# Performance work log

Measured on AMD Instinct MI355X. Metric: run time of the kernel, lower is better.

## Reference

```python
import jax, jax.numpy as jnp
import numpy as np

N = 50000   # nodes per graph
E = 500000  # edges per graph
F_IN = 128  # num_features
H = 128     # hidden_channels
C = 64      # num_classes
G = 64      # graphs per batch
NEG_SLOPE = 0.2


def setup_inputs() -> dict:
    key = jax.random.key(0)
    ks = jax.random.split(key, 16)
    s = 1.0 / np.sqrt(H)
    return {
        "x1": jax.random.normal(ks[0], (N, F_IN), jnp.float32),
        "x2": jax.random.normal(ks[1], (N, F_IN), jnp.float32),
        # stacked params for the 2 GATConv layers (F_IN == H so shapes match)
        "convW": jax.random.normal(ks[2], (2, H, H), jnp.float32) * s,
        "att_src": jax.random.normal(ks[3], (2, H), jnp.float32) * s,
        "att_dst": jax.random.normal(ks[4], (2, H), jnp.float32) * s,
        "conv_b": jnp.zeros((2, H), jnp.float32),
        "mlp_w1": jax.random.normal(ks[5], (H, H), jnp.float32) * s,
        "mlp_b1": jnp.zeros((H,), jnp.float32),
        "mlp_w2": jax.random.normal(ks[6], (H, C), jnp.float32) * s,
        "mlp_b2": jnp.zeros((C,), jnp.float32),
        "edge_index1": jax.random.randint(ks[7], (2, E), 0, N, jnp.int64),
        "batch1": jnp.sort(jax.random.randint(ks[8], (N,), 0, G, jnp.int64)),
        "edge_index2": jax.random.randint(ks[9], (2, E), 0, N, jnp.int64),
        "batch2": jnp.sort(jax.random.randint(ks[10], (N,), 0, G, jnp.int64)),
    }


def gat_conv(x, src, dst, W, a_s, a_d, b):
    # PyG GATConv, heads=1, add_self_loops already applied in src/dst
    n = x.shape[0]
    h = x @ W                                   # [N, H]
    alpha_s = h @ a_s                           # [N]
    alpha_d = h @ a_d                           # [N]
    e = alpha_s[src] + alpha_d[dst]             # [Etot]
    e = jnp.where(e > 0, e, NEG_SLOPE * e)      # leaky_relu
    # segment softmax over incoming edges of each dst node
    m = jax.ops.segment_max(e, dst, num_segments=n)
    ex = jnp.exp(e - m[dst])
    denom = jax.ops.segment_sum(ex, dst, num_segments=n)
    alpha = ex / denom[dst]                     # [Etot]
    out = jax.ops.segment_sum(h[src] * alpha[:, None], dst, num_segments=n)
    return out + b


def reference(x1, x2, convW, att_src, att_dst, conv_b,
              mlp_w1, mlp_b1, mlp_w2, mlp_b2,
              edge_index1, batch1, edge_index2, batch2):
    def branch(x, ei):
        n = x.shape[0]
        loops = jnp.arange(n, dtype=ei.dtype)
        src = jnp.concatenate([ei[0], loops])
        dst = jnp.concatenate([ei[1], loops])
        # num_layers=3 -> 2 convs; i != num_layers-1 always true -> ELU after each
        for l in range(2):
            x = gat_conv(x, src, dst, convW[l], att_src[l], att_dst[l], conv_b[l])
            x = jax.nn.elu(x)
            # dropout p=0.5 is identity in eval mode
        return jax.nn.relu(x @ mlp_w1 + mlp_b1) @ mlp_w2 + mlp_b2

    h1 = branch(x1, edge_index1)
    h2 = branch(x2, edge_index2)
    p1 = jax.ops.segment_sum(h1, batch1, num_segments=G)  # [G, C]
    p2 = jax.ops.segment_sum(h2, batch2, num_segments=G)  # [G, C]
    return p1.T @ p2                                      # [C, C]
```

## Files before the change

### kernel.cpp

```cpp
#include <hip/hip_runtime.h>
#include <cstdint>
#include <cstddef>

#define NNODES 50000
#define NEDGES 500000
#define NTOT (NEDGES + NNODES)
#define HDIM 128
#define CDIM 64
#define GDIM 64
#define NB 250
#define NPB 200
#define CHUNK 2048
#define NCHB ((NEDGES + CHUNK - 1) / CHUNK)

typedef __bf16 bf16x8 __attribute__((ext_vector_type(8)));
typedef __bf16 bf16x2 __attribute__((ext_vector_type(2)));
typedef float f32x4 __attribute__((ext_vector_type(4)));


__global__ __launch_bounds__(256) void k_setup(const float* __restrict__ convW,
                                               const float* __restrict__ w1,
                                               const float* __restrict__ w2,
                                               const float* __restrict__ a_s,
                                               const float* __restrict__ a_d,
                                               __bf16* __restrict__ WtC,
                                               __bf16* __restrict__ Wt1,
                                               __bf16* __restrict__ Wt2,
                                               float* __restrict__ Wa,
                                               float* __restrict__ p) {
    int b = blockIdx.x, tid = threadIdx.x;
    if (b < 128) {
        int i = b * 256 + tid;
        int mat = i >> 14, rem = i & 16383;
        int k = rem >> 7, n = rem & 127;
        WtC[mat * 16384 + n * 128 + k] = (__bf16)convW[i];
    } else if (b < 192) {
        int i = (b - 128) * 256 + tid;
        int k = i >> 7, n = i & 127;
        Wt1[n * 128 + k] = (__bf16)w1[i];
    } else if (b < 224) {
        int i = (b - 192) * 256 + tid;
        int k = i >> 6, n = i & 63;
        Wt2[n * 128 + k] = (__bf16)w2[i];
    } else if (b == 224) {
        for (int o = tid; o < 512; o += 256) {
            int l = o >> 8, r = o & 255;
            int type = r >> 7, k = r & 127;
            const float* a = (type ? a_d : a_s) + l * 128;
            const float* Wrow = convW + l * 16384 + k * 128;
            float s = 0.f;
            for (int j = 0; j < 128; j++) s += Wrow[j] * a[j];
            Wa[o] = s;
        }
    } else {
        for (int i = tid; i < 2 * GDIM * CDIM; i += 256) p[i] = 0.f;
    }
}


__global__ __launch_bounds__(256) void k_bhist(const int* __restrict__ ei0,
                                               const int* __restrict__ ei1,
                                               int* __restrict__ bcntB, int e) {
    __shared__ int h[NB];
    const int* dst = (blockIdx.y ? ei1 : ei0) + NEDGES;
    int* bcnt = bcntB + blockIdx.y * NB;
    for (int t = threadIdx.x; t < NB; t += 256) h[t] = 0;
    __syncthreads();
    int base = blockIdx.x * CHUNK;
    int lim = min(base + CHUNK, e);
    for (int i = base + threadIdx.x; i < lim; i += 256) atomicAdd(&h[dst[i] / NPB], 1);
    __syncthreads();
    for (int t = threadIdx.x; t < NB; t += 256)
        if (h[t]) atomicAdd(&bcnt[t], h[t]);
}

__global__ __launch_bounds__(256) void k_bscan(const int* __restrict__ bcntB,
                                               int* __restrict__ boffB,
                                               int* __restrict__ bcurB) {
    __shared__ int s[256];
    int t = threadIdx.x;
    const int* bcnt = bcntB + blockIdx.y * NB;
    int* boff = boffB + blockIdx.y * (NB + 1);
    int* bcur = bcurB + blockIdx.y * NB;
    int v = (t < NB) ? bcnt[t] : 0;
    s[t] = v;
    __syncthreads();
    for (int off = 1; off < 256; off <<= 1) {
        int x = (t >= off) ? s[t - off] : 0;
        __syncthreads();
        s[t] += x;
        __syncthreads();
    }
    if (t < NB) {
        boff[t + 1] = s[t];
        bcur[t] = s[t] - v;
        if (t == 0) boff[0] = 0;
    }
}

__global__ __launch_bounds__(256) void k_part(const int* __restrict__ ei0,
                                              const int* __restrict__ ei1,
                                              int* __restrict__ bcurB,
                                              int2* __restrict__ partB, int e) {
    __shared__ int cnt[NB], boffL[NB], gbase[NB], cur2[NB];
    __shared__ int tmp[256];
    __shared__ int2 staged[CHUNK];
    const int* eis = blockIdx.y ? ei1 : ei0;
    int* bcur = bcurB + blockIdx.y * NB;
    int2* part = partB + blockIdx.y * (size_t)NEDGES;
    int t = threadIdx.x;
    for (int i = t; i < NB; i += 256) { cnt[i] = 0; cur2[i] = 0; }
    __syncthreads();
    int base = blockIdx.x * CHUNK;
    int lim = min(base + CHUNK, e);
    int nloc = lim - base;

    int s_[8], d_[8], b_[8];
    bool v_[8];
#pragma unroll
    for (int k = 0; k < 8; k++) {
        int i = base + k * 256 + t;
        v_[k] = i < lim;
        s_[k] = 0; d_[k] = 0; b_[k] = 0;
        if (v_[k]) {
            s_[k] = eis[i];
            d_[k] = eis[NEDGES + i];
            b_[k] = d_[k] / NPB;
            atomicAdd(&cnt[b_[k]], 1);
        }
    }
    __syncthreads();
    tmp[t] = (t < NB) ? cnt[t] : 0;
    __syncthreads();
    for (int off = 1; off < 256; off <<= 1) {
        int x = (t >= off) ? tmp[t - off] : 0;
        __syncthreads();
        tmp[t] += x;
        __syncthreads();
    }
    if (t < NB) boffL[t] = tmp[t] - cnt[t];
    __syncthreads();
    if (t < NB) {
        int c = cnt[t];
        gbase[t] = c ? atomicAdd(&bcur[t], c) : 0;
    }
    __syncthreads();
#pragma unroll
    for (int k = 0; k < 8; k++) {
        if (v_[k]) {
            int pos = atomicAdd(&cur2[b_[k]], 1);
            staged[boffL[b_[k]] + pos] = make_int2(s_[k], d_[k]);
        }
    }
    __syncthreads();
    for (int i = t; i < nloc; i += 256) {
        int2 r = staged[i];
        int b = r.y / NPB;
        part[gbase[b] + (i - boffL[b])] = r;
    }
}

__global__ __launch_bounds__(256) void k_bdeg(const int2* __restrict__ partB,
                                              const int* __restrict__ boffB,
                                              int* __restrict__ degB, size_t sN) {
    __shared__ int h[NPB];
    int b = blockIdx.x;
    const int* boff = boffB + blockIdx.y * (NB + 1);
    const int2* part = partB + blockIdx.y * (size_t)NEDGES;
    int* deg = degB + blockIdx.y * sN;
    int t = threadIdx.x;
    if (t < NPB) h[t] = 0;
    __syncthreads();
    int beg = boff[b], end = boff[b + 1];
    int n0 = b * NPB;
    for (int i = beg + t; i < end; i += 256) atomicAdd(&h[part[i].y - n0], 1);
    __syncthreads();
    if (t < NPB) deg[n0 + t] = h[t];
}

__device__ inline int block_scan_incl(int v, int* lds) {
    int lane = threadIdx.x & 63, wid = threadIdx.x >> 6;
#pragma unroll
    for (int off = 1; off < 64; off <<= 1) {
        int nv = __shfl_up(v, off);
        if (lane >= off) v += nv;
    }
    if (lane == 63) lds[wid] = v;
    __syncthreads();
    if (wid == 0) {
        int s = (lane < 16) ? lds[lane] : 0;
#pragma unroll
        for (int off = 1; off < 16; off <<= 1) {
            int nv = __shfl_up(s, off);
            if (lane >= off) s += nv;
        }
        if (lane < 16) lds[lane] = s;
    }
    __syncthreads();
    return (wid > 0) ? v + lds[wid - 1] : v;
}

__global__ __launch_bounds__(1024) void k_scan1(const int* __restrict__ degB, int* __restrict__ inclB,
                                                int* __restrict__ bsumsB, size_t sN, int n) {
    __shared__ int lds[16];
    const int* deg = degB + blockIdx.y * sN;
    int* incl = inclB + blockIdx.y * sN;
    int* bsums = bsumsB + blockIdx.y * 64;
    int i = blockIdx.x * 1024 + threadIdx.x;
    int v = (i < n) ? deg[i] : 0;
    int s = block_scan_incl(v, lds);
    if (i < n) incl[i] = s;
    if (threadIdx.x == 1023) bsums[blockIdx.x] = s;
}

__global__ void k_scan2(int* __restrict__ bsumsB, int nb) {
    int* bsums = bsumsB + blockIdx.y * 64;
    int lane = threadIdx.x;
    int v = (lane < nb) ? bsums[lane] : 0;
#pragma unroll
    for (int off = 1; off < 64; off <<= 1) {
        int nv = __shfl_up(v, off);
        if (lane >= off) v += nv;
    }
    if (lane < nb) bsums[lane] = v;
}

__global__ __launch_bounds__(1024) void k_scan3(const int* __restrict__ inclB,
                                                const int* __restrict__ bsumsB, int* __restrict__ rpB,
                                                size_t sN, size_t sNp1, int n) {
    int i = blockIdx.x * 1024 + threadIdx.x;
    if (i >= n) return;
    const int* incl = inclB + blockIdx.y * sN;
    const int* bsums = bsumsB + blockIdx.y * 64;
    int* row_ptr = rpB + blockIdx.y * sNp1;
    int off = (blockIdx.x > 0) ? bsums[blockIdx.x - 1] : 0;
    row_ptr[i + 1] = incl[i] + off + i + 1;
    if (i == 0) row_ptr[0] = 0;
}

__global__ __launch_bounds__(256) void k_place(const int2* __restrict__ partB,
                                               const int* __restrict__ boffB,
                                               const int* __restrict__ rpB, size_t sNp1,
                                               int* __restrict__ colB, size_t sE) {
    __shared__ int cur[NPB];
    int b = blockIdx.x;
    const int* boff = boffB + blockIdx.y * (NB + 1);
    const int2* part = partB + blockIdx.y * (size_t)NEDGES;
    const int* row_ptr = rpB + blockIdx.y * sNp1;
    int* col = colB + blockIdx.y * sE;
    int t = threadIdx.x;
    int n0 = b * NPB;
    if (t < NPB) {
        int rp = row_ptr[n0 + t];
        cur[t] = rp + 1;
        col[rp] = n0 + t;
    }
    __syncthreads();
    int beg = boff[b], end = boff[b + 1];
    for (int i = beg + t; i < end; i += 256) {
        int2 r = part[i];
        int p = atomicAdd(&cur[r.y - n0], 1);
        col[p] = r.x;
    }
}


template <bool AF32>
__global__ __launch_bounds__(256) void k_gemm_conv(const float* __restrict__ x0,
                                                   const float* __restrict__ x1,
                                                   const __bf16* __restrict__ Ab, size_t As_,
                                                   const __bf16* __restrict__ Wt,
                                                   const float* __restrict__ Was,
                                                   const float* __restrict__ Wad,
                                                   float* __restrict__ asB, float* __restrict__ adB,
                                                   size_t aS,
                                                   __bf16* __restrict__ OutB, size_t Os_, int M) {
    constexpr int BN = 128;
    __shared__ __align__(16) unsigned short As[64][136];
    __shared__ __align__(16) unsigned short Bs[BN][136];
    const int tid = threadIdx.x;
    const int lane = tid & 63, w = tid >> 6;
    const int row0 = blockIdx.x * 64;
    __bf16* Out = OutB + blockIdx.y * Os_;

#pragma unroll
    for (int t = 0; t < 4; t++) {
        int ch = t * 256 + tid;
        int r = ch >> 4, cx = ch & 15;
        int grow = row0 + r;
        bf16x8 v = {};
        if (grow < M) {
            if (AF32) {
                const float* Ap = (blockIdx.y ? x1 : x0) + (size_t)grow * 128 + cx * 8;
                float4 f0 = *reinterpret_cast<const float4*>(Ap);
                float4 f1 = *reinterpret_cast<const float4*>(Ap + 4);
                v[0] = (__bf16)f0.x; v[1] = (__bf16)f0.y; v[2] = (__bf16)f0.z; v[3] = (__bf16)f0.w;
                v[4] = (__bf16)f1.x; v[5] = (__bf16)f1.y; v[6] = (__bf16)f1.z; v[7] = (__bf16)f1.w;
            } else {
                v = *reinterpret_cast<const bf16x8*>(Ab + blockIdx.y * As_ + (size_t)grow * 128 + cx * 8);
            }
        }
        *reinterpret_cast<bf16x8*>(&As[r][cx * 8]) = v;
    }
#pragma unroll
    for (int t = 0; t < 8; t++) {
        int ch = t * 256 + tid;
        int r = ch >> 4, cx = ch & 15;
        bf16x8 v = *reinterpret_cast<const bf16x8*>(Wt + (size_t)r * 128 + cx * 8);
        *reinterpret_cast<bf16x8*>(&Bs[r][cx * 8]) = v;
    }
    __syncthreads();

    {
        int row = tid >> 2, seg = tid & 3;
        float ss = 0.f, sd = 0.f;
#pragma unroll
        for (int k = 0; k < 32; k++) {
            int kk = seg * 32 + k;
            float a = __int_as_float(((unsigned)As[row][kk]) << 16);
            ss += a * Was[kk];
            sd += a * Wad[kk];
        }
        ss += __shfl_xor(ss, 1); ss += __shfl_xor(ss, 2);
        sd += __shfl_xor(sd, 1); sd += __shfl_xor(sd, 2);
        if (seg == 0) {
            int grow = row0 + row;
            if (grow < M) {
                (asB + blockIdx.y * aS)[grow] = ss;
                (adB + blockIdx.y * aS)[grow] = sd;
            }
        }
    }

    const int wr0 = (w >> 1) * 32;
    const int wc0 = (w & 1) * 64;
    f32x4 acc[2][4] = {};

#pragma unroll
    for (int ks = 0; ks < 4; ks++) {
        const int koff = ks * 32 + (lane >> 4) * 8;
        bf16x8 af[2], bfr[4];
#pragma unroll
        for (int mf = 0; mf < 2; mf++)
            af[mf] = *reinterpret_cast<const bf16x8*>(&As[wr0 + mf * 16 + (lane & 15)][koff]);
#pragma unroll
        for (int nf = 0; nf < 4; nf++)
            bfr[nf] = *reinterpret_cast<const bf16x8*>(&Bs[wc0 + nf * 16 + (lane & 15)][koff]);
#pragma unroll
        for (int mf = 0; mf < 2; mf++)
#pragma unroll
            for (int nf = 0; nf < 4; nf++)
                acc[mf][nf] = __builtin_amdgcn_mfma_f32_16x16x32_bf16(af[mf], bfr[nf], acc[mf][nf], 0, 0, 0);
    }

#pragma unroll
    for (int mf = 0; mf < 2; mf++) {
#pragma unroll
        for (int r = 0; r < 4; r++) {
            int row = row0 + wr0 + mf * 16 + (lane >> 4) * 4 + r;
            if (row >= M) continue;
#pragma unroll
            for (int nf = 0; nf < 4; nf++) {
                int colc = wc0 + nf * 16 + (lane & 15);
                Out[(size_t)row * BN + colc] = (__bf16)acc[mf][nf][r];
            }
        }
    }
}


__global__ __launch_bounds__(256) void k_gat_agg(const __bf16* __restrict__ hB, size_t hS,
                                                 const float* __restrict__ asB,
                                                 const float* __restrict__ adB, size_t aS,
                                                 const int* __restrict__ rpB, size_t sNp1,
                                                 const int* __restrict__ colB, size_t sE,
                                                 const float* __restrict__ bias,
                                                 __bf16* __restrict__ outB, size_t oS, int n) {
    int node = blockIdx.x * 4 + (threadIdx.x >> 6);
    int lane = threadIdx.x & 63;
    if (node >= n) return;
    const float* alpha_s = asB + blockIdx.y * aS;
    const int* row_ptr = rpB + blockIdx.y * sNp1;
    const int* col = colB + blockIdx.y * sE;
    const char* hbase = (const char*)(hB + blockIdx.y * hS);
    float ad = (adB + blockIdx.y * aS)[node];
    int beg = row_ptr[node], end = row_ptr[node + 1];
    int deg = end - beg;
    int sub = lane >> 4, fo = lane & 15;
    int foff = fo * 16;

    float acc[8] = {0.f, 0.f, 0.f, 0.f, 0.f, 0.f, 0.f, 0.f};

    if (deg <= 64) {
        bool v = lane < deg;
        int c = 0;
        float e = -1e30f;
        if (v) {
            c = col[beg + lane];
            e = alpha_s[c] + ad;
            e = (e > 0.f) ? e : 0.2f * e;
        }
        float m = e;
#pragma unroll
        for (int off = 32; off; off >>= 1) m = fmaxf(m, __shfl_xor(m, off));
        float ex = v ? __expf(e - m) : 0.f;
        float den = ex;
#pragma unroll
        for (int off = 32; off; off >>= 1) den += __shfl_xor(den, off);
        float wn = ex / den;

        int nIter = (deg + 3) >> 2;
        int k = sub;
        for (int t = 0; t < nIter; t += 2) {
            int k1 = k & 63, k2 = (k + 4) & 63;
            int c1 = __shfl(c, k1); float w1 = __shfl(wn, k1);
            int c2 = __shfl(c, k2); float w2 = __shfl(wn, k2);
            bool v1 = k < deg, v2 = (k + 4) < deg;
            w1 = v1 ? w1 : 0.f; c1 = v1 ? c1 : 0;
            w2 = v2 ? w2 : 0.f; c2 = v2 ? c2 : 0;
            bf16x8 h1 = *reinterpret_cast<const bf16x8*>(hbase + (c1 << 8) + foff);
            bf16x8 h2 = *reinterpret_cast<const bf16x8*>(hbase + (c2 << 8) + foff);
#pragma unroll
            for (int q = 0; q < 8; q++) acc[q] += w1 * (float)h1[q] + w2 * (float)h2[q];
            k += 8;
        }
    } else {
        float m = -1e30f;
        for (int i = beg + lane; i < end; i += 64) {
            float e = alpha_s[col[i]] + ad;
            e = (e > 0.f) ? e : 0.2f * e;
            m = fmaxf(m, e);
        }
#pragma unroll
        for (int off = 32; off; off >>= 1) m = fmaxf(m, __shfl_xor(m, off));
        float den = 0.f;
        for (int i = beg + lane; i < end; i += 64) {
            float e = alpha_s[col[i]] + ad;
            e = (e > 0.f) ? e : 0.2f * e;
            den += __expf(e - m);
        }
#pragma unroll
        for (int off = 32; off; off >>= 1) den += __shfl_xor(den, off);
        float rinv = 1.f / den;
        for (int i = beg + sub; i < end; i += 4) {
            int cc = col[i];
            float e = alpha_s[cc] + ad;
            e = (e > 0.f) ? e : 0.2f * e;
            float wv = __expf(e - m) * rinv;
            bf16x8 hv = *reinterpret_cast<const bf16x8*>(hbase + (cc << 8) + foff);
#pragma unroll
            for (int q = 0; q < 8; q++) acc[q] += wv * (float)hv[q];
        }
    }

#pragma unroll
    for (int q = 0; q < 8; q++) {
        acc[q] += __shfl_xor(acc[q], 16);
        acc[q] += __shfl_xor(acc[q], 32);
    }
    float2 bv = *reinterpret_cast<const float2*>(bias + fo * 8 + 2 * sub);
    float x0 = (sub & 2) ? ((sub & 1) ? acc[6] : acc[4]) : ((sub & 1) ? acc[2] : acc[0]);
    float x1 = (sub & 2) ? ((sub & 1) ? acc[7] : acc[5]) : ((sub & 1) ? acc[3] : acc[1]);
    x0 += bv.x; x1 += bv.y;
    x0 = (x0 > 0.f) ? x0 : __expf(x0) - 1.f;
    x1 = (x1 > 0.f) ? x1 : __expf(x1) - 1.f;
    bf16x2 ov;
    ov.x = (__bf16)x0; ov.y = (__bf16)x1;
    char* ob = (char*)(outB + blockIdx.y * oS) + ((unsigned)node << 8) + foff + sub * 4;
    *reinterpret_cast<unsigned int*>(ob) = __builtin_bit_cast(unsigned int, ov);
}


__global__ __launch_bounds__(256) void k_mlp_pool(const __bf16* __restrict__ AbB, size_t As_,
                                                  const __bf16* __restrict__ Wt1,
                                                  const __bf16* __restrict__ Wt2,
                                                  const float* __restrict__ b1,
                                                  const float* __restrict__ b2,
                                                  const int* __restrict__ bat0,
                                                  const int* __restrict__ bat1,
                                                  float* __restrict__ pB, size_t pS, int M) {
    __shared__ __align__(16) unsigned short As[64][136];
    __shared__ __align__(16) unsigned short Bs[128][136];
    const int tid = threadIdx.x;
    const int lane = tid & 63, w = tid >> 6;
    const int row0 = blockIdx.x * 64;
    const __bf16* Ab = AbB + blockIdx.y * As_;
    const int* batch = blockIdx.y ? bat1 : bat0;
    float* p = pB + blockIdx.y * pS;

#pragma unroll
    for (int t = 0; t < 4; t++) {
        int ch = t * 256 + tid;
        int r = ch >> 4, cx = ch & 15;
        int grow = row0 + r;
        bf16x8 v = {};
        if (grow < M) v = *reinterpret_cast<const bf16x8*>(Ab + (size_t)grow * 128 + cx * 8);
        *reinterpret_cast<bf16x8*>(&As[r][cx * 8]) = v;
    }
#pragma unroll
    for (int t = 0; t < 8; t++) {
        int ch = t * 256 + tid;
        int r = ch >> 4, cx = ch & 15;
        bf16x8 v = *reinterpret_cast<const bf16x8*>(Wt1 + (size_t)r * 128 + cx * 8);
        *reinterpret_cast<bf16x8*>(&Bs[r][cx * 8]) = v;
    }
    __syncthreads();

    {
        const int wr0 = (w >> 1) * 32;
        const int wc0 = (w & 1) * 64;
        f32x4 acc[2][4] = {};
#pragma unroll
        for (int ks = 0; ks < 4; ks++) {
            const int koff = ks * 32 + (lane >> 4) * 8;
            bf16x8 af[2], bfr[4];
#pragma unroll
            for (int mf = 0; mf < 2; mf++)
                af[mf] = *reinterpret_cast<const bf16x8*>(&As[wr0 + mf * 16 + (lane & 15)][koff]);
#pragma unroll
            for (int nf = 0; nf < 4; nf++)
                bfr[nf] = *reinterpret_cast<const bf16x8*>(&Bs[wc0 + nf * 16 + (lane & 15)][koff]);
#pragma unroll
            for (int mf = 0; mf < 2; mf++)
#pragma unroll
                for (int nf = 0; nf < 4; nf++)
                    acc[mf][nf] = __builtin_amdgcn_mfma_f32_16x16x32_bf16(af[mf], bfr[nf], acc[mf][nf], 0, 0, 0);
        }
        __syncthreads();
#pragma unroll
        for (int mf = 0; mf < 2; mf++)
#pragma unroll
            for (int r = 0; r < 4; r++) {
                int row = wr0 + mf * 16 + (lane >> 4) * 4 + r;
#pragma unroll
                for (int nf = 0; nf < 4; nf++) {
                    int colc = wc0 + nf * 16 + (lane & 15);
                    float v = fmaxf(acc[mf][nf][r] + b1[colc], 0.f);
                    As[row][colc] = __builtin_bit_cast(unsigned short, (__bf16)v);
                }
            }
#pragma unroll
        for (int t = 0; t < 4; t++) {
            int ch = t * 256 + tid;
            int r = ch >> 4, cx = ch & 15;
            bf16x8 v = *reinterpret_cast<const bf16x8*>(Wt2 + (size_t)r * 128 + cx * 8);
            *reinterpret_cast<bf16x8*>(&Bs[r][cx * 8]) = v;
        }
        __syncthreads();
    }

    const int wr2 = w * 16;
    f32x4 acc2[4] = {};
#pragma unroll
    for (int ks = 0; ks < 4; ks++) {
        const int koff = ks * 32 + (lane >> 4) * 8;
        bf16x8 a2 = *reinterpret_cast<const bf16x8*>(&As[wr2 + (lane & 15)][koff]);
#pragma unroll
        for (int nf = 0; nf < 4; nf++) {
            bf16x8 bf2 = *reinterpret_cast<const bf16x8*>(&Bs[nf * 16 + (lane & 15)][koff]);
            acc2[nf] = __builtin_amdgcn_mfma_f32_16x16x32_bf16(a2, bf2, acc2[nf], 0, 0, 0);
        }
    }

    int q = lane >> 4, c = lane & 15;
    bool full = (row0 + 63) < M;
    int g0 = batch[min(row0, M - 1)];
    int g1 = batch[min(row0 + 63, M - 1)];
    if (full && g0 == g1) {
        float s0 = acc2[0][0] + acc2[0][1] + acc2[0][2] + acc2[0][3];
        float s1 = acc2[1][0] + acc2[1][1] + acc2[1][2] + acc2[1][3];
        float s2 = acc2[2][0] + acc2[2][1] + acc2[2][2] + acc2[2][3];
        float s3 = acc2[3][0] + acc2[3][1] + acc2[3][2] + acc2[3][3];
        s0 += __shfl_xor(s0, 16); s0 += __shfl_xor(s0, 32);
        s1 += __shfl_xor(s1, 16); s1 += __shfl_xor(s1, 32);
        s2 += __shfl_xor(s2, 16); s2 += __shfl_xor(s2, 32);
        s3 += __shfl_xor(s3, 16); s3 += __shfl_xor(s3, 32);
        float v = (q & 2) ? ((q & 1) ? s3 : s2) : ((q & 1) ? s1 : s0);
        v += 16.f * b2[q * 16 + c];
        atomicAdd(&p[g0 * CDIM + q * 16 + c], v);
    } else {
        float b2v[4];
#pragma unroll
        for (int nf = 0; nf < 4; nf++) b2v[nf] = b2[nf * 16 + c];
#pragma unroll
        for (int r = 0; r < 4; r++) {
            int row = row0 + wr2 + q * 4 + r;
            if (row >= M) continue;
            int g = batch[row];
#pragma unroll
            for (int nf = 0; nf < 4; nf++)
                atomicAdd(&p[g * CDIM + nf * 16 + c], acc2[nf][r] + b2v[nf]);
        }
    }
}


__global__ __launch_bounds__(64) void k_final(const float* __restrict__ p, float* __restrict__ out) {
    int i = blockIdx.x;
    int j = threadIdx.x;
    const float* p1 = p;
    const float* p2 = p + GDIM * CDIM;
    float s = 0.f;
    for (int g = 0; g < GDIM; ++g) s += p1[g * CDIM + i] * p2[g * CDIM + j];
    out[i * CDIM + j] = s;
}


static inline size_t align_up(size_t x, size_t a) { return (x + a - 1) & ~(a - 1); }

struct Ws {
    __bf16 *Hb, *Yb;
    __bf16 *WtC, *Wt1, *Wt2;
    float *alpha_s, *alpha_d, *Wa, *p;
    int *deg, *incl, *row_ptr, *bsums, *col;
    int *bcnt, *boff, *bcur;
    int2* part;
    size_t sNH, sN, sNp1, sE;
    size_t need;
};

static Ws carve(void* ws, bool combined) {
    char* p = (char*)ws;
    size_t off = 0;
    Ws w;
    int nb = combined ? 2 : 1;
    auto take = [&](size_t bytes) {
        char* r = p + off;
        off = align_up(off + bytes, 256);
        return r;
    };
    w.Hb = (__bf16*)take((size_t)nb * NNODES * HDIM * 2);
    w.Yb = (__bf16*)take((size_t)nb * NNODES * HDIM * 2);
    w.alpha_s = (float*)take((size_t)nb * NNODES * 4);
    w.alpha_d = (float*)take((size_t)nb * NNODES * 4);
    w.col = (int*)take((size_t)nb * NTOT * 4);
    w.part = (int2*)take((size_t)nb * NEDGES * 8);
    w.deg = (int*)take((size_t)nb * NNODES * 4);
    w.incl = (int*)take((size_t)nb * NNODES * 4);
    w.row_ptr = (int*)take((size_t)nb * (NNODES + 1) * 4);
    w.bsums = (int*)take((size_t)2 * 64 * 4);
    w.bcnt = (int*)take((size_t)2 * NB * 4);
    w.boff = (int*)take((size_t)2 * (NB + 1) * 4);
    w.bcur = (int*)take((size_t)2 * NB * 4);
    w.WtC = (__bf16*)take((size_t)2 * HDIM * HDIM * 2);
    w.Wt1 = (__bf16*)take((size_t)HDIM * HDIM * 2);
    w.Wt2 = (__bf16*)take((size_t)HDIM * CDIM * 2);
    w.Wa = (float*)take((size_t)512 * 4);
    w.p = (float*)take((size_t)2 * GDIM * CDIM * 4);
    w.need = off;
    size_t s = combined ? 1 : 0;
    w.sNH = s * (size_t)NNODES * HDIM;
    w.sN = s * (size_t)NNODES;
    w.sNp1 = s * (size_t)(NNODES + 1);
    w.sE = s * (size_t)NTOT;
    return w;
}

static void pipeline(const Ws& w, const float* xA, const float* xB,
                     const int* eiA, const int* eiB,
                     const int* batA, const int* batB,
                     const float* conv_b, const float* b1, const float* b2,
                     float* pbase, size_t pstride, int yc, hipStream_t stream) {
    const int N = NNODES, E = NEDGES;
    int nb = (N + 1023) / 1024;
    dim3 gC(NCHB, yc), gB(NB, yc), g1(1, yc), gS(nb, yc);
    dim3 gW((N + 3) / 4, yc);
    dim3 gG((N + 63) / 64, yc);

    hipMemsetAsync(w.bcnt, 0, (size_t)yc * NB * 4, stream);
    k_bhist<<<gC, 256, 0, stream>>>(eiA, eiB, w.bcnt, E);
    k_bscan<<<g1, 256, 0, stream>>>(w.bcnt, w.boff, w.bcur);
    k_part<<<gC, 256, 0, stream>>>(eiA, eiB, w.bcur, w.part, E);
    k_bdeg<<<gB, 256, 0, stream>>>(w.part, w.boff, w.deg, w.sN);
    k_scan1<<<gS, 1024, 0, stream>>>(w.deg, w.incl, w.bsums, w.sN, N);
    k_scan2<<<g1, 64, 0, stream>>>(w.bsums, nb);
    k_scan3<<<gS, 1024, 0, stream>>>(w.incl, w.bsums, w.row_ptr, w.sN, w.sNp1, N);
    k_place<<<gB, 256, 0, stream>>>(w.part, w.boff, w.row_ptr, w.sNp1, w.col, w.sE);

    k_gemm_conv<true><<<gG, 256, 0, stream>>>(
        xA, xB, nullptr, 0, w.WtC, w.Wa, w.Wa + 128,
        w.alpha_s, w.alpha_d, w.sN, w.Hb, w.sNH, N);
    k_gat_agg<<<gW, 256, 0, stream>>>(w.Hb, w.sNH, w.alpha_s, w.alpha_d, w.sN,
                                      w.row_ptr, w.sNp1, w.col, w.sE, conv_b, w.Yb, w.sNH, N);
    k_gemm_conv<false><<<gG, 256, 0, stream>>>(
        nullptr, nullptr, w.Yb, w.sNH, w.WtC + HDIM * HDIM, w.Wa + 256, w.Wa + 384,
        w.alpha_s, w.alpha_d, w.sN, w.Hb, w.sNH, N);
    k_gat_agg<<<gW, 256, 0, stream>>>(w.Hb, w.sNH, w.alpha_s, w.alpha_d, w.sN,
                                      w.row_ptr, w.sNp1, w.col, w.sE, conv_b + HDIM, w.Yb, w.sNH, N);
    k_mlp_pool<<<gG, 256, 0, stream>>>(w.Yb, w.sNH, w.Wt1, w.Wt2, b1, b2,
                                       batA, batB, pbase, pstride, N);
}

extern "C" void kernel_launch(void* const* d_in, const int* in_sizes, int n_in, void* d_out,
                              int out_size, void* d_ws, size_t ws_size, hipStream_t stream) {
    const float* x1      = (const float*)d_in[0];
    const float* x2      = (const float*)d_in[1];
    const float* convW   = (const float*)d_in[2];
    const float* att_src = (const float*)d_in[3];
    const float* att_dst = (const float*)d_in[4];
    const float* conv_b  = (const float*)d_in[5];
    const float* mlp_w1  = (const float*)d_in[6];
    const float* mlp_b1  = (const float*)d_in[7];
    const float* mlp_w2  = (const float*)d_in[8];
    const float* mlp_b2  = (const float*)d_in[9];
    const int* ei1       = (const int*)d_in[10];
    const int* batch1    = (const int*)d_in[11];
    const int* ei2       = (const int*)d_in[12];
    const int* batch2    = (const int*)d_in[13];
    float* out = (float*)d_out;

    Ws wc = carve(d_ws, true);
    bool combined = ws_size >= wc.need;
    Ws w = combined ? wc : carve(d_ws, false);

    k_setup<<<226, 256, 0, stream>>>(convW, mlp_w1, mlp_w2, att_src, att_dst,
                                     w.WtC, w.Wt1, w.Wt2, w.Wa, w.p);

    if (combined) {
        pipeline(w, x1, x2, ei1, ei2, batch1, batch2, conv_b,
                 mlp_b1, mlp_b2, w.p, (size_t)GDIM * CDIM, 2, stream);
    } else {
        pipeline(w, x1, x1, ei1, ei1, batch1, batch1, conv_b,
                 mlp_b1, mlp_b2, w.p, 0, 1, stream);
        pipeline(w, x2, x2, ei2, ei2, batch2, batch2, conv_b,
                 mlp_b1, mlp_b2, w.p + GDIM * CDIM, 0, 1, stream);
    }

    k_final<<<CDIM, 64, 0, stream>>>(w.p, out);
}
```

Before: 347.0 us.

## Fuse CSR degree/scan/placement into one kernel and use 16-lane groups per node

Merges the degree histogram, three-pass global scan and edge placement into a single per-bucket kernel. The bucket offset from the partition scan serves as the global prefix, and a local block scan computes row pointers. This removes four launches and their intermediate buffers. Separately, GAT aggregation now gives each node a 16-lane group instead of a full wavefront, with each lane owning 8 features, which removes the cross-subgroup shuffle reduction but serializes edges per node.

```diff
diff --git a/kernel.cpp b/kernel.cpp
--- a/kernel.cpp
+++ b/kernel.cpp
@@ -160,106 +160,53 @@
     }
 }
 
-__global__ __launch_bounds__(256) void k_bdeg(const int2* __restrict__ partB,
-                                              const int* __restrict__ boffB,
-                                              int* __restrict__ degB, size_t sN) {
+__global__ __launch_bounds__(256) void k_place(const int2* __restrict__ partB,
+                                               const int* __restrict__ boffB,
+                                               int* __restrict__ rpB, size_t sNp1,
+                                               int* __restrict__ colB, size_t sE) {
     __shared__ int h[NPB];
+    __shared__ int lds4[4];
     int b = blockIdx.x;
     const int* boff = boffB + blockIdx.y * (NB + 1);
     const int2* part = partB + blockIdx.y * (size_t)NEDGES;
-    int* deg = degB + blockIdx.y * sN;
-    int t = threadIdx.x;
-    if (t < NPB) h[t] = 0;
-    __syncthreads();
-    int beg = boff[b], end = boff[b + 1];
-    int n0 = b * NPB;
-    for (int i = beg + t; i < end; i += 256) atomicAdd(&h[part[i].y - n0], 1);
-    __syncthreads();
-    if (t < NPB) deg[n0 + t] = h[t];
-}
-
-__device__ inline int block_scan_incl(int v, int* lds) {
-    int lane = threadIdx.x & 63, wid = threadIdx.x >> 6;
-#pragma unroll
-    for (int off = 1; off < 64; off <<= 1) {
-        int nv = __shfl_up(v, off);
-        if (lane >= off) v += nv;
-    }
-    if (lane == 63) lds[wid] = v;
-    __syncthreads();
-    if (wid == 0) {
-        int s = (lane < 16) ? lds[lane] : 0;
-#pragma unroll
-        for (int off = 1; off < 16; off <<= 1) {
-            int nv = __shfl_up(s, off);
-            if (lane >= off) s += nv;
-        }
-        if (lane < 16) lds[lane] = s;
-    }
-    __syncthreads();
-    return (wid > 0) ? v + lds[wid - 1] : v;
-}
-
-__global__ __launch_bounds__(1024) void k_scan1(const int* __restrict__ degB, int* __restrict__ inclB,
-                                                int* __restrict__ bsumsB, size_t sN, int n) {
-    __shared__ int lds[16];
-    const int* deg = degB + blockIdx.y * sN;
-    int* incl = inclB + blockIdx.y * sN;
-    int* bsums = bsumsB + blockIdx.y * 64;
-    int i = blockIdx.x * 1024 + threadIdx.x;
-    int v = (i < n) ? deg[i] : 0;
-    int s = block_scan_incl(v, lds);
-    if (i < n) incl[i] = s;
-    if (threadIdx.x == 1023) bsums[blockIdx.x] = s;
-}
-
-__global__ void k_scan2(int* __restrict__ bsumsB, int nb) {
-    int* bsums = bsumsB + blockIdx.y * 64;
-    int lane = threadIdx.x;
-    int v = (lane < nb) ? bsums[lane] : 0;
-#pragma unroll
-    for (int off = 1; off < 64; off <<= 1) {
-        int nv = __shfl_up(v, off);
-        if (lane >= off) v += nv;
-    }
-    if (lane < nb) bsums[lane] = v;
-}
-
-__global__ __launch_bounds__(1024) void k_scan3(const int* __restrict__ inclB,
-                                                const int* __restrict__ bsumsB, int* __restrict__ rpB,
-                                                size_t sN, size_t sNp1, int n) {
-    int i = blockIdx.x * 1024 + threadIdx.x;
-    if (i >= n) return;
-    const int* incl = inclB + blockIdx.y * sN;
-    const int* bsums = bsumsB + blockIdx.y * 64;
     int* row_ptr = rpB + blockIdx.y * sNp1;
-    int off = (blockIdx.x > 0) ? bsums[blockIdx.x - 1] : 0;
-    row_ptr[i + 1] = incl[i] + off + i + 1;
-    if (i == 0) row_ptr[0] = 0;
-}
-
-__global__ __launch_bounds__(256) void k_place(const int2* __restrict__ partB,
-                                               const int* __restrict__ boffB,
-                                               const int* __restrict__ rpB, size_t sNp1,
-                                               int* __restrict__ colB, size_t sE) {
-    __shared__ int cur[NPB];
-    int b = blockIdx.x;
-    const int* boff = boffB + blockIdx.y * (NB + 1);
-    const int2* part = partB + blockIdx.y * (size_t)NEDGES;
-    const int* row_ptr = rpB + blockIdx.y * sNp1;
     int* col = colB + blockIdx.y * sE;
     int t = threadIdx.x;
     int n0 = b * NPB;
+    if (t < NPB) h[t] = 0;
+    __syncthreads();
+    int beg = boff[b], end = boff[b + 1];
+    for (int i = beg + t; i < end; i += 256) atomicAdd(&h[part[i].y - n0], 1);
+    __syncthreads();
+    int v = (t < NPB) ? h[t] : 0;
+    int lane = t & 63, wid = t >> 6;
+    int incl = v;
+#pragma unroll
+    for (int off = 1; off < 64; off <<= 1) {
+        int nv = __shfl_up(incl, off);
+        if (lane >= off) incl += nv;
+    }
+    if (lane == 63) lds4[wid] = incl;
+    __syncthreads();
+    if (t == 0) {
+        int s = 0;
+#pragma unroll
+        for (int j = 0; j < 4; j++) { s += lds4[j]; lds4[j] = s; }
+    }
+    __syncthreads();
+    if (wid > 0) incl += lds4[wid - 1];
     if (t < NPB) {
-        int rp = row_ptr[n0 + t];
-        cur[t] = rp + 1;
-        col[rp] = n0 + t;
-    }
-    __syncthreads();
-    int beg = boff[b], end = boff[b + 1];
+        int rp_end = beg + n0 + incl + t + 1;
+        row_ptr[n0 + t + 1] = rp_end;
+        int rp_start = rp_end - v - 1;
+        col[rp_start] = n0 + t;
+        h[t] = rp_start + 1;
+        if (b == 0 && t == 0) row_ptr[0] = 0;
+    }
+    __syncthreads();
     for (int i = beg + t; i < end; i += 256) {
         int2 r = part[i];
-        int p = atomicAdd(&cur[r.y - n0], 1);
+        int p = atomicAdd(&h[r.y - n0], 1);
         col[p] = r.x;
     }
 }
@@ -376,8 +323,9 @@
                                                  const int* __restrict__ colB, size_t sE,
                                                  const float* __restrict__ bias,
                                                  __bf16* __restrict__ outB, size_t oS, int n) {
-    int node = blockIdx.x * 4 + (threadIdx.x >> 6);
-    int lane = threadIdx.x & 63;
+    int grp = threadIdx.x >> 4;
+    int node = blockIdx.x * 16 + grp;
+    int l = threadIdx.x & 15;
     if (node >= n) return;
     const float* alpha_s = asB + blockIdx.y * aS;
     const int* row_ptr = rpB + blockIdx.y * sNp1;
@@ -386,88 +334,81 @@
     float ad = (adB + blockIdx.y * aS)[node];
     int beg = row_ptr[node], end = row_ptr[node + 1];
     int deg = end - beg;
-    int sub = lane >> 4, fo = lane & 15;
-    int foff = fo * 16;
+    int foff = l * 16;
 
     float acc[8] = {0.f, 0.f, 0.f, 0.f, 0.f, 0.f, 0.f, 0.f};
 
-    if (deg <= 64) {
-        bool v = lane < deg;
+    if (deg <= 16) {
+        bool v = l < deg;
         int c = 0;
         float e = -1e30f;
         if (v) {
-            c = col[beg + lane];
-            e = alpha_s[c] + ad;
-            e = (e > 0.f) ? e : 0.2f * e;
+            c = col[beg + l];
+            float t = alpha_s[c] + ad;
+            e = (t > 0.f) ? t : 0.2f * t;
         }
         float m = e;
 #pragma unroll
-        for (int off = 32; off; off >>= 1) m = fmaxf(m, __shfl_xor(m, off));
+        for (int off = 8; off; off >>= 1) m = fmaxf(m, __shfl_xor(m, off));
         float ex = v ? __expf(e - m) : 0.f;
         float den = ex;
 #pragma unroll
-        for (int off = 32; off; off >>= 1) den += __shfl_xor(den, off);
+        for (int off = 8; off; off >>= 1) den += __shfl_xor(den, off);
         float wn = ex / den;
 
-        int nIter = (deg + 3) >> 2;
-        int k = sub;
-        for (int t = 0; t < nIter; t += 2) {
-            int k1 = k & 63, k2 = (k + 4) & 63;
-            int c1 = __shfl(c, k1); float w1 = __shfl(wn, k1);
-            int c2 = __shfl(c, k2); float w2 = __shfl(wn, k2);
-            bool v1 = k < deg, v2 = (k + 4) < deg;
-            w1 = v1 ? w1 : 0.f; c1 = v1 ? c1 : 0;
-            w2 = v2 ? w2 : 0.f; c2 = v2 ? c2 : 0;
-            bf16x8 h1 = *reinterpret_cast<const bf16x8*>(hbase + (c1 << 8) + foff);
-            bf16x8 h2 = *reinterpret_cast<const bf16x8*>(hbase + (c2 << 8) + foff);
-#pragma unroll
-            for (int q = 0; q < 8; q++) acc[q] += w1 * (float)h1[q] + w2 * (float)h2[q];
-            k += 8;
+        int base = (grp << 4) & 63;
+        for (int e2 = 0; e2 < deg; e2 += 2) {
+            int i1 = base + e2, i2 = base + e2 + 1;
+            int s1 = __shfl(c, i1); float w1 = __shfl(wn, i1);
+            int s2 = __shfl(c, i2); float w2 = __shfl(wn, i2);
+            bool h2v = (e2 + 1) < deg;
+            s2 = h2v ? s2 : s1;
+            w2 = h2v ? w2 : 0.f;
+            bf16x8 h1 = *reinterpret_cast<const bf16x8*>(hbase + ((size_t)(unsigned)s1 << 8) + foff);
+            bf16x8 hh2 = *reinterpret_cast<const bf16x8*>(hbase + ((size_t)(unsigned)s2 << 8) + foff);
+#pragma unroll
+            for (int q = 0; q < 8; q++) acc[q] += w1 * (float)h1[q] + w2 * (float)hh2[q];
         }
     } else {
         float m = -1e30f;
-        for (int i = beg + lane; i < end; i += 64) {
-            float e = alpha_s[col[i]] + ad;
-            e = (e > 0.f) ? e : 0.2f * e;
-            m = fmaxf(m, e);
-        }
-#pragma unroll
-        for (int off = 32; off; off >>= 1) m = fmaxf(m, __shfl_xor(m, off));
+        for (int i = beg + l; i < end; i += 16) {
+            float t = alpha_s[col[i]] + ad;
+            t = (t > 0.f) ? t : 0.2f * t;
+            m = fmaxf(m, t);
+        }
+#pragma unroll
+        for (int off = 8; off; off >>= 1) m = fmaxf(m, __shfl_xor(m, off));
         float den = 0.f;
-        for (int i = beg + lane; i < end; i += 64) {
-            float e = alpha_s[col[i]] + ad;
-            e = (e > 0.f) ? e : 0.2f * e;
-            den += __expf(e - m);
-        }
-#pragma unroll
-        for (int off = 32; off; off >>= 1) den += __shfl_xor(den, off);
+        for (int i = beg + l; i < end; i += 16) {
+            float t = alpha_s[col[i]] + ad;
+            t = (t > 0.f) ? t : 0.2f * t;
+            den += __expf(t - m);
+        }
+#pragma unroll
+        for (int off = 8; off; off >>= 1) den += __shfl_xor(den, off);
         float rinv = 1.f / den;
-        for (int i = beg + sub; i < end; i += 4) {
-            int cc = col[i];
-            float e = alpha_s[cc] + ad;
-            e = (e > 0.f) ? e : 0.2f * e;
-            float wv = __expf(e - m) * rinv;
-            bf16x8 hv = *reinterpret_cast<const bf16x8*>(hbase + (cc << 8) + foff);
+        for (int e2 = beg; e2 < end; e2++) {
+            int cc = col[e2];
+            float t = alpha_s[cc] + ad;
+            t = (t > 0.f) ? t : 0.2f * t;
+            float wv = __expf(t - m) * rinv;
+            bf16x8 hv = *reinterpret_cast<const bf16x8*>(hbase + ((size_t)(unsigned)cc << 8) + foff);
 #pragma unroll
             for (int q = 0; q < 8; q++) acc[q] += wv * (float)hv[q];
         }
     }
 
+    float4 b0 = *reinterpret_cast<const float4*>(bias + l * 8);
+    float4 b1 = *reinterpret_cast<const float4*>(bias + l * 8 + 4);
+    float bb[8] = {b0.x, b0.y, b0.z, b0.w, b1.x, b1.y, b1.z, b1.w};
+    bf16x8 o;
 #pragma unroll
     for (int q = 0; q < 8; q++) {
-        acc[q] += __shfl_xor(acc[q], 16);
-        acc[q] += __shfl_xor(acc[q], 32);
-    }
-    float2 bv = *reinterpret_cast<const float2*>(bias + fo * 8 + 2 * sub);
-    float x0 = (sub & 2) ? ((sub & 1) ? acc[6] : acc[4]) : ((sub & 1) ? acc[2] : acc[0]);
-    float x1 = (sub & 2) ? ((sub & 1) ? acc[7] : acc[5]) : ((sub & 1) ? acc[3] : acc[1]);
-    x0 += bv.x; x1 += bv.y;
-    x0 = (x0 > 0.f) ? x0 : __expf(x0) - 1.f;
-    x1 = (x1 > 0.f) ? x1 : __expf(x1) - 1.f;
-    bf16x2 ov;
-    ov.x = (__bf16)x0; ov.y = (__bf16)x1;
-    char* ob = (char*)(outB + blockIdx.y * oS) + ((unsigned)node << 8) + foff + sub * 4;
-    *reinterpret_cast<unsigned int*>(ob) = __builtin_bit_cast(unsigned int, ov);
+        float x = acc[q] + bb[q];
+        x = (x > 0.f) ? x : __expf(x) - 1.f;
+        o[q] = (__bf16)x;
+    }
+    *reinterpret_cast<bf16x8*>((char*)(outB + blockIdx.y * oS) + ((size_t)(unsigned)node << 8) + foff) = o;
 }
 
 
@@ -612,7 +553,7 @@
     __bf16 *Hb, *Yb;
     __bf16 *WtC, *Wt1, *Wt2;
     float *alpha_s, *alpha_d, *Wa, *p;
-    int *deg, *incl, *row_ptr, *bsums, *col;
+    int *row_ptr, *col;
     int *bcnt, *boff, *bcur;
     int2* part;
     size_t sNH, sN, sNp1, sE;
@@ -635,10 +576,7 @@
     w.alpha_d = (float*)take((size_t)nb * NNODES * 4);
     w.col = (int*)take((size_t)nb * NTOT * 4);
     w.part = (int2*)take((size_t)nb * NEDGES * 8);
-    w.deg = (int*)take((size_t)nb * NNODES * 4);
-    w.incl = (int*)take((size_t)nb * NNODES * 4);
     w.row_ptr = (int*)take((size_t)nb * (NNODES + 1) * 4);
-    w.bsums = (int*)take((size_t)2 * 64 * 4);
     w.bcnt = (int*)take((size_t)2 * NB * 4);
     w.boff = (int*)take((size_t)2 * (NB + 1) * 4);
     w.bcur = (int*)take((size_t)2 * NB * 4);
@@ -662,19 +600,14 @@
                      const float* conv_b, const float* b1, const float* b2,
                      float* pbase, size_t pstride, int yc, hipStream_t stream) {
     const int N = NNODES, E = NEDGES;
-    int nb = (N + 1023) / 1024;
-    dim3 gC(NCHB, yc), gB(NB, yc), g1(1, yc), gS(nb, yc);
-    dim3 gW((N + 3) / 4, yc);
+    dim3 gC(NCHB, yc), gB(NB, yc), g1(1, yc);
+    dim3 gW((N + 15) / 16, yc);
     dim3 gG((N + 63) / 64, yc);
 
     hipMemsetAsync(w.bcnt, 0, (size_t)yc * NB * 4, stream);
     k_bhist<<<gC, 256, 0, stream>>>(eiA, eiB, w.bcnt, E);
     k_bscan<<<g1, 256, 0, stream>>>(w.bcnt, w.boff, w.bcur);
     k_part<<<gC, 256, 0, stream>>>(eiA, eiB, w.bcur, w.part, E);
-    k_bdeg<<<gB, 256, 0, stream>>>(w.part, w.boff, w.deg, w.sN);
-    k_scan1<<<gS, 1024, 0, stream>>>(w.deg, w.incl, w.bsums, w.sN, N);
-    k_scan2<<<g1, 64, 0, stream>>>(w.bsums, nb);
-    k_scan3<<<gS, 1024, 0, stream>>>(w.incl, w.bsums, w.row_ptr, w.sN, w.sNp1, N);
     k_place<<<gB, 256, 0, stream>>>(w.part, w.boff, w.row_ptr, w.sNp1, w.col, w.sE);
 
     k_gemm_conv<true><<<gG, 256, 0, stream>>>(
```

Result: no change. 346.9 us (-0.0%).
